# Optimization experiments

Hardware: AMD Instinct MI355X
Metric: run time of the kernel (lower is better)

## Reference

```python
import jax, jax.numpy as jnp
import numpy as np

N = 50000          # total nodes (2 types x 25000)
E = 400000         # edges
NEG = 0.2          # leaky_relu negative slope


def _seg_softmax(e, dst, n):
    # softmax over edges grouped by destination node
    m = jax.ops.segment_max(e, dst, num_segments=n)
    m = jnp.where(jnp.isfinite(m), m, 0.0)
    ex = jnp.exp(e - m[dst])
    s = jax.ops.segment_sum(ex, dst, num_segments=n)
    return ex / (s[dst] + 1e-16)


def _gat_conv(h, src, dst, W, al, ar, b, heads, out, res=None, act=None):
    n = h.shape[0]
    ft = (h @ W).reshape(n, heads, out)               # [N,H,D]
    el = jnp.sum(ft * al, axis=-1)                    # [N,H]
    er = jnp.sum(ft * ar, axis=-1)                    # [N,H]
    e = jax.nn.leaky_relu(el[src] + er[dst], NEG)     # [E,H]
    alpha = _seg_softmax(e, dst, n)                   # [E,H]
    rst = jax.ops.segment_sum(ft[src] * alpha[:, :, None], dst, num_segments=n)
    if isinstance(res, str):                          # identity residual (in == heads*out)
        rst = rst + h.reshape(n, heads, out)
    elif res is not None:                             # linear residual projection
        rst = rst + (h @ res).reshape(n, heads, out)
    rst = rst + b                                     # bias [H,D]
    if act is not None:
        rst = act(rst)
    return rst


def setup_inputs() -> dict:
    key = jax.random.key(0)
    ks = jax.random.split(key, 24)
    g = lambda i, shp, s=0.05: jax.random.normal(ks[i], shp, jnp.float32) * s
    inp = {
        "x0": jax.random.normal(ks[0], (25000, 256), jnp.float32),
        "x1": jax.random.normal(ks[1], (25000, 256), jnp.float32),
        "src": jax.random.randint(ks[2], (E,), 0, N, jnp.int32).astype(jnp.int64),
        "dst": jax.random.randint(ks[3], (E,), 0, N, jnp.int32).astype(jnp.int64),
        # per-type input projections
        "fc0_W": g(4, (256, 64)), "fc0_b": jnp.zeros((64,), jnp.float32),
        "fc1_W": g(5, (256, 64)), "fc1_b": jnp.zeros((64,), jnp.float32),
        # layer 0: 64 -> 8 heads x 64
        "W0": g(6, (64, 512)), "al0": g(7, (8, 64)), "ar0": g(8, (8, 64)), "b0": jnp.zeros((8, 64), jnp.float32),
        # layer 1: 512 -> 8 heads x 64 (identity residual)
        "W1": g(9, (512, 512)), "al1": g(10, (8, 64)), "ar1": g(11, (8, 64)), "b1": jnp.zeros((8, 64), jnp.float32),
        # output layer: 512 -> 1 head x 16 (linear residual)
        "W2": g(12, (512, 16)), "al2": g(13, (1, 16)), "ar2": g(14, (1, 16)), "b2": jnp.zeros((1, 16), jnp.float32),
        "resW2": g(15, (512, 16)),
    }
    return inp


def reference(x0, x1, src, dst, fc0_W, fc0_b, fc1_W, fc1_b,
              W0, al0, ar0, b0, W1, al1, ar1, b1,
              W2, al2, ar2, b2, resW2):
    # per-type linear projections, then concat over node axis
    h = jnp.concatenate([x0 @ fc0_W + fc0_b, x1 @ fc1_W + fc1_b], axis=0)  # [N,64]
    h = _gat_conv(h, src, dst, W0, al0, ar0, b0, 8, 64, None, jax.nn.elu).reshape(N, -1)
    h = _gat_conv(h, src, dst, W1, al1, ar1, b1, 8, 64, "id", jax.nn.elu).reshape(N, -1)
    encoded = h
    logits = _gat_conv(h, src, dst, W2, al2, ar2, b2, 1, 16, resW2, None).mean(axis=1)  # [N,16]
    return (logits, encoded)
```

## Files before the change

kernel.cpp:

```cpp
#include <hip/hip_runtime.h>
#include <hip/hip_bf16.h>
#include <math.h>

typedef __hip_bfloat16 bf16;
typedef __attribute__((ext_vector_type(8))) short short8;
typedef __attribute__((ext_vector_type(8))) unsigned short ushort8;
typedef __attribute__((ext_vector_type(4))) float floatx4;

#define NNODES 50000
#define NHALF  25000
#define NEDGES 400000
#define NEG_SLOPE 0.2f

__device__ __forceinline__ float b2f(bf16 x){ return __bfloat162float(x); }
__device__ __forceinline__ bf16  f2b(float x){ return __float2bfloat16(x); }
__device__ __forceinline__ float u2f(unsigned short u){ return __uint_as_float(((unsigned)u) << 16); }

__device__ __forceinline__ float loadF(const void* p, long i, int f32){
  return f32 ? ((const float*)p)[i] : b2f(((const bf16*)p)[i]);
}
__device__ __forceinline__ void storeOut(void* p, long i, float v, int f32){
  if (f32) ((float*)p)[i] = v; else ((bf16*)p)[i] = f2b(v);
}

__device__ __forceinline__ unsigned fenc(float f){
  unsigned b = __float_as_uint(f);
  return (b & 0x80000000u) ? ~b : (b | 0x80000000u);
}
__device__ __forceinline__ float fdec(unsigned k){
  unsigned b = (k & 0x80000000u) ? (k & 0x7fffffffu) : ~k;
  return __uint_as_float(b);
}

__device__ __forceinline__ void gl_lds16(const bf16* g, short* l){
  __builtin_amdgcn_global_load_lds(
      (const __attribute__((address_space(1))) unsigned int*)g,
      (__attribute__((address_space(3))) unsigned int*)l, 16, 0, 0);
}

__global__ void k_detect(const unsigned short* __restrict__ x0u,
                         const unsigned* __restrict__ dstu,
                         int* __restrict__ flags)
{
  __shared__ int sh_insane;
  __shared__ unsigned sh_or;
  if (threadIdx.x == 0) { sh_insane = 0; sh_or = 0u; }
  __syncthreads();
  int insane = 0; unsigned orv = 0u;
  for (int i = threadIdx.x; i < 2048; i += 256) {
    unsigned short w = x0u[2 * i];
    int ex = (w >> 7) & 0xFF;
    if (w != 0 && (ex < 108 || ex > 142)) insane++;
    orv |= dstu[2 * i + 1];
  }
  atomicAdd(&sh_insane, insane);
  atomicOr(&sh_or, orv);
  __syncthreads();
  if (threadIdx.x == 0) {
    flags[0] = (sh_insane > 512) ? 1 : 0;
    flags[1] = (sh_or == 0u) ? 1 : 0;
  }
}

__global__ void k_conv_idx(const int* __restrict__ sraw, const int* __restrict__ draw,
                           int* __restrict__ s32, int* __restrict__ d32,
                           int* __restrict__ deg,
                           const int* __restrict__ flags)
{
  int e = blockIdx.x * blockDim.x + threadIdx.x;
  if (e >= NEDGES) return;
  int stride = flags[1] ? 2 : 1;
  int s = sraw[(long)e * stride];
  int d = draw[(long)e * stride];
  s32[e] = s;
  d32[e] = d;
  atomicAdd(&deg[d], 1);
}

struct WSrc { const void* p[17]; void* dst[17]; int n[17]; int M[17]; int st[17]; };

__global__ void k_canon(WSrc w, const int* __restrict__ flags, int total)
{
  int f32 = flags[0];
  for (int t = blockIdx.x * blockDim.x + threadIdx.x; t < total;
       t += gridDim.x * blockDim.x) {
    int idx = t, k = 0;
    while (idx >= w.n[k]) { idx -= w.n[k]; k++; }
    bf16 v = f2b(loadF(w.p[k], idx, f32));
    if (w.M[k] == 0) {
      ((bf16*)w.dst[k])[idx] = v;
    } else {
      int m = idx % w.M[k], kk = idx / w.M[k];
      ((bf16*)w.dst[k])[(long)m * w.st[k] + kk] = v;
    }
  }
}

__global__ void k_convx(const void* __restrict__ x0, const void* __restrict__ x1,
                        bf16* __restrict__ xb, const int* __restrict__ flags)
{
  long t = (long)(blockIdx.x * blockDim.x + threadIdx.x) * 8;
  if (t >= (long)NNODES * 256) return;
  long half = (long)NHALF * 256;
  const void* src = (t < half) ? x0 : x1;
  long off = (t < half) ? t : t - half;
  short8 o;
  if (flags[0]) {
    const float* f = (const float*)src + off;
    floatx4 a = *(const floatx4*)f;
    floatx4 b = *(const floatx4*)(f + 4);
    #pragma unroll
    for (int j = 0; j < 4; ++j) {
      bf16 x = f2b(a[j]); o[j] = *(short*)&x;
      bf16 y = f2b(b[j]); o[j + 4] = *(short*)&y;
    }
  } else {
    o = *(const short8*)((const bf16*)src + off);
  }
  *(short8*)(xb + t) = o;
}

__global__ __launch_bounds__(256) void k_gemm_mfma(
    const bf16* __restrict__ A, const bf16* __restrict__ Wt,
    bf16* __restrict__ C, int N, int K, int ldc, int Mout,
    const bf16* __restrict__ bias,
    const bf16* __restrict__ al, const bf16* __restrict__ ar,
    float* __restrict__ elOut, float* __restrict__ erOut,
    unsigned* __restrict__ Menc)
{
  __shared__ __align__(16) short lsA[128 * 32];
  __shared__ __align__(16) short lsB[128 * 32];
  __shared__ unsigned sMaxE[2], sMaxR[2];
  int tid = threadIdx.x;
  int wave = tid >> 6, lane = tid & 63;
  int wm = wave >> 1, wn = wave & 1;
  int rowBase = blockIdx.x * 128;
  int colBase = blockIdx.y * 128;

  if (tid < 2) { sMaxE[tid] = 0u; sMaxR[tid] = 0u; }

  floatx4 acc[4][4] = {};
  int laneRow = lane >> 2;
  int laneCol = (lane & 3) * 8;
  int cA0 = wave * 2, cA1 = cA0 + 1;

  for (int kb = 0; kb < K; kb += 32) {
    int r0 = rowBase + cA0 * 16 + laneRow; if (r0 > N - 1) r0 = N - 1;
    int r1 = rowBase + cA1 * 16 + laneRow; if (r1 > N - 1) r1 = N - 1;
    gl_lds16(A + (size_t)r0 * K + kb + laneCol, &lsA[cA0 * 512]);
    gl_lds16(A + (size_t)r1 * K + kb + laneCol, &lsA[cA1 * 512]);
    int m0 = colBase + cA0 * 16 + laneRow;
    int m1 = colBase + cA1 * 16 + laneRow;
    gl_lds16(Wt + (size_t)m0 * K + kb + laneCol, &lsB[cA0 * 512]);
    gl_lds16(Wt + (size_t)m1 * K + kb + laneCol, &lsB[cA1 * 512]);
    __syncthreads();

    short8 af[4], bfr[4];
    int lr = lane & 15, q8 = (lane >> 4) * 8;
    #pragma unroll
    for (int mt = 0; mt < 4; ++mt)
      af[mt] = *(const short8*)&lsA[(wm * 64 + mt * 16 + lr) * 32 + q8];
    #pragma unroll
    for (int nt = 0; nt < 4; ++nt)
      bfr[nt] = *(const short8*)&lsB[(wn * 64 + nt * 16 + lr) * 32 + q8];
    #pragma unroll
    for (int mt = 0; mt < 4; ++mt)
      #pragma unroll
      for (int nt = 0; nt < 4; ++nt)
        acc[mt][nt] = __builtin_amdgcn_mfma_f32_16x16x32_bf16(
            af[mt], bfr[nt], acc[mt][nt], 0, 0, 0);
    __syncthreads();
  }

  int lc = lane & 15, rq = (lane >> 4) * 4;
  #pragma unroll
  for (int mt = 0; mt < 4; ++mt) {
    #pragma unroll
    for (int nt = 0; nt < 4; ++nt) {
      int col = colBase + wn * 64 + nt * 16 + lc;
      if (col >= Mout) continue;
      float bsv = bias ? b2f(bias[col]) : 0.f;
      #pragma unroll
      for (int r = 0; r < 4; ++r) {
        int row = rowBase + wm * 64 + mt * 16 + rq + r;
        if (row < N) C[(size_t)row * ldc + col] = f2b(acc[mt][nt][r] + bsv);
      }
    }
  }

  if (elOut) {
    int h = (colBase >> 6) + wn;
    float alv[4], arv[4];
    #pragma unroll
    for (int nt = 0; nt < 4; ++nt) {
      alv[nt] = b2f(al[h * 64 + nt * 16 + lc]);
      arv[nt] = b2f(ar[h * 64 + nt * 16 + lc]);
    }
    float mael = -1e30f, maer = -1e30f;
    #pragma unroll
    for (int mt = 0; mt < 4; ++mt) {
      #pragma unroll
      for (int r = 0; r < 4; ++r) {
        float pe = acc[mt][0][r] * alv[0] + acc[mt][1][r] * alv[1]
                 + acc[mt][2][r] * alv[2] + acc[mt][3][r] * alv[3];
        float pr = acc[mt][0][r] * arv[0] + acc[mt][1][r] * arv[1]
                 + acc[mt][2][r] * arv[2] + acc[mt][3][r] * arv[3];
        #pragma unroll
        for (int off = 1; off < 16; off <<= 1) {
          pe += __shfl_xor(pe, off);
          pr += __shfl_xor(pr, off);
        }
        int row = rowBase + wm * 64 + mt * 16 + rq + r;
        if (row < N) {
          if (lc == 0) { elOut[row * 8 + h] = pe; erOut[row * 8 + h] = pr; }
          mael = fmaxf(mael, pe);
          maer = fmaxf(maer, pr);
        }
      }
    }
    #pragma unroll
    for (int off = 16; off < 64; off <<= 1) {
      mael = fmaxf(mael, __shfl_xor(mael, off));
      maer = fmaxf(maer, __shfl_xor(maer, off));
    }
    if (lane == 0) {
      atomicMax(&sMaxE[wn], fenc(mael));
      atomicMax(&sMaxR[wn], fenc(maer));
    }
    __syncthreads();
    if (tid < 2) {
      int h0 = colBase >> 6;
      atomicMax(&Menc[h0 + tid], sMaxE[tid]);
      atomicMax(&Menc[8 + h0 + tid], sMaxR[tid]);
    }
  }
}

__global__ __launch_bounds__(256) void k_elr1(
    const bf16* __restrict__ ft2,
    const bf16* __restrict__ al, const bf16* __restrict__ ar,
    float* __restrict__ el, float* __restrict__ er,
    unsigned* __restrict__ Menc)
{
  __shared__ float rA[4], rB[4];
  int tid = threadIdx.x;
  int n = blockIdx.x * 256 + tid;
  float a = -1e30f, b = -1e30f;
  if (n < NNODES) {
    const unsigned short* f = (const unsigned short*)ft2 + (size_t)n * 32;
    float aa = 0.f, bb = 0.f;
    #pragma unroll
    for (int d = 0; d < 16; ++d) {
      float x = u2f(f[d]);
      aa += x * b2f(al[d]);
      bb += x * b2f(ar[d]);
    }
    a = aa; b = bb;
    el[n] = a; er[n] = b;
  }
  #pragma unroll
  for (int off = 1; off <= 32; off <<= 1) {
    a = fmaxf(a, __shfl_xor(a, off));
    b = fmaxf(b, __shfl_xor(b, off));
  }
  int wave = tid >> 6, lane = tid & 63;
  if (lane == 0) { rA[wave] = a; rB[wave] = b; }
  __syncthreads();
  if (tid == 0) {
    float ma = -1e30f, mb = -1e30f;
    #pragma unroll
    for (int w2 = 0; w2 < 4; ++w2) { ma = fmaxf(ma, rA[w2]); mb = fmaxf(mb, rB[w2]); }
    atomicMax(&Menc[0], fenc(ma));
    atomicMax(&Menc[1], fenc(mb));
  }
}

__global__ __launch_bounds__(1024) void k_bsum(const int* __restrict__ deg,
                                               int* __restrict__ bsum, int n)
{
  __shared__ int ws[16];
  int tid = threadIdx.x, lane = tid & 63, wv = tid >> 6;
  int i = blockIdx.x * 1024 + tid;
  int v = (i < n) ? deg[i] : 0;
  #pragma unroll
  for (int off = 1; off < 64; off <<= 1) v += __shfl_xor(v, off);
  if (lane == 0) ws[wv] = v;
  __syncthreads();
  if (tid < 16) {
    int s = ws[tid];
    #pragma unroll
    for (int off = 1; off < 16; off <<= 1) s += __shfl_xor(s, off);
    if (tid == 0) bsum[blockIdx.x] = s;
  }
}

__global__ void k_bscan(int* __restrict__ bsum, int* __restrict__ row_start,
                        int nb, int n)
{
  int lane = threadIdx.x;
  int v = (lane < nb) ? bsum[lane] : 0;
  int x = v;
  #pragma unroll
  for (int off = 1; off < 64; off <<= 1) {
    int y = __shfl_up(x, off);
    if (lane >= off) x += y;
  }
  if (lane < nb) bsum[lane] = x - v;
  if (lane == 63) row_start[n] = x;
}

__global__ __launch_bounds__(1024) void k_scan2(const int* __restrict__ deg,
                                                const int* __restrict__ boff,
                                                int* __restrict__ row_start,
                                                int* __restrict__ cursor, int n)
{
  __shared__ int ws[16];
  int tid = threadIdx.x, lane = tid & 63, wv = tid >> 6;
  int i = blockIdx.x * 1024 + tid;
  int v = (i < n) ? deg[i] : 0;
  int x = v;
  #pragma unroll
  for (int off = 1; off < 64; off <<= 1) {
    int y = __shfl_up(x, off);
    if (lane >= off) x += y;
  }
  if (lane == 63) ws[wv] = x;
  __syncthreads();
  if (wv == 0 && lane < 16) {
    int s = ws[lane];
    int xs = s;
    #pragma unroll
    for (int off = 1; off < 16; off <<= 1) {
      int y = __shfl_up(xs, off);
      if (lane >= off) xs += y;
    }
    ws[lane] = xs - s;
  }
  __syncthreads();
  if (i < n) {
    int val = boff[blockIdx.x] + ws[wv] + x - v;
    row_start[i] = val;
    cursor[i] = val;
  }
}

__global__ void k_fill(const int* __restrict__ src, const int* __restrict__ dst,
                       int* __restrict__ cursor, int* __restrict__ csr_src, int E)
{
  int e = blockIdx.x * blockDim.x + threadIdx.x;
  if (e < E) {
    int p = atomicAdd(&cursor[dst[e]], 1);
    csr_src[p] = src[e];
  }
}

__global__ __launch_bounds__(256) void k_agg8(
    const int* __restrict__ row_start, const int* __restrict__ csr_src,
    const float* __restrict__ el, const float* __restrict__ er,
    const unsigned* __restrict__ Menc,
    const bf16* __restrict__ ft, const bf16* __restrict__ hin,
    const bf16* __restrict__ bias,
    bf16* __restrict__ hout, void* __restrict__ dout, long dout_off,
    const int* __restrict__ flags, int mode)
{
  int wv = (int)((blockIdx.x * blockDim.x + threadIdx.x) >> 6);
  int lane = threadIdx.x & 63;
  if (wv >= NNODES) return;
  int n = wv, g = lane >> 3;
  int st = row_start[n], en = row_start[n + 1];
  float mm = fdec(Menc[g]) + fdec(Menc[8 + g]);
  float Mh = mm > 0.f ? mm : NEG_SLOPE * mm;
  float ern = er[n * 8 + g];

  const unsigned short* ftS = (const unsigned short*)ft;
  float ssum = 0.f;
  float acc[8] = {};
  int i = st;
  for (; i + 4 <= en; i += 4) {
    int sn0 = csr_src[i],     sn1 = csr_src[i + 1];
    int sn2 = csr_src[i + 2], sn3 = csr_src[i + 3];
    float e0 = el[sn0 * 8 + g], e1 = el[sn1 * 8 + g];
    float e2 = el[sn2 * 8 + g], e3 = el[sn3 * 8 + g];
    ushort8 r0 = *(const ushort8*)&ftS[(size_t)sn0 * 512 + lane * 8];
    ushort8 r1 = *(const ushort8*)&ftS[(size_t)sn1 * 512 + lane * 8];
    ushort8 r2 = *(const ushort8*)&ftS[(size_t)sn2 * 512 + lane * 8];
    ushort8 r3 = *(const ushort8*)&ftS[(size_t)sn3 * 512 + lane * 8];
    float v0 = e0 + ern, v1 = e1 + ern, v2 = e2 + ern, v3 = e3 + ern;
    v0 = v0 > 0.f ? v0 : NEG_SLOPE * v0;
    v1 = v1 > 0.f ? v1 : NEG_SLOPE * v1;
    v2 = v2 > 0.f ? v2 : NEG_SLOPE * v2;
    v3 = v3 > 0.f ? v3 : NEG_SLOPE * v3;
    float w0 = __expf(v0 - Mh), w1 = __expf(v1 - Mh);
    float w2 = __expf(v2 - Mh), w3 = __expf(v3 - Mh);
    ssum += (w0 + w1) + (w2 + w3);
    #pragma unroll
    for (int j = 0; j < 8; ++j)
      acc[j] += (w0 * u2f(r0[j]) + w1 * u2f(r1[j]))
              + (w2 * u2f(r2[j]) + w3 * u2f(r3[j]));
  }
  for (; i < en; ++i) {
    int sn = csr_src[i];
    float v0 = el[sn * 8 + g] + ern;
    v0 = v0 > 0.f ? v0 : NEG_SLOPE * v0;
    float w0 = __expf(v0 - Mh);
    ushort8 r0 = *(const ushort8*)&ftS[(size_t)sn * 512 + lane * 8];
    ssum += w0;
    #pragma unroll
    for (int j = 0; j < 8; ++j)
      acc[j] += w0 * u2f(r0[j]);
  }

  float inv = ssum > 0.f ? 1.f / ssum : 0.f;
  int f32 = flags[0];
  short8 outv;
  float rr[8];
  #pragma unroll
  for (int j = 0; j < 8; ++j) {
    int col = lane * 8 + j;
    float r = acc[j] * inv + b2f(bias[col]);
    if (mode == 1) r += b2f(hin[(size_t)n * 512 + col]);
    r = r > 0.f ? r : expm1f(r);
    rr[j] = r;
    bf16 o = f2b(r);
    outv[j] = *(short*)&o;
  }
  *(short8*)&hout[(size_t)n * 512 + lane * 8] = outv;
  if (dout) {
    if (f32) {
      floatx4 o0, o1;
      #pragma unroll
      for (int j = 0; j < 4; ++j) { o0[j] = rr[j]; o1[j] = rr[j + 4]; }
      float* dp = (float*)dout + dout_off + (size_t)n * 512 + lane * 8;
      __builtin_nontemporal_store(o0, (floatx4*)dp);
      __builtin_nontemporal_store(o1, (floatx4*)(dp + 4));
    } else {
      __builtin_nontemporal_store(outv,
          (short8*)&((bf16*)dout)[dout_off + (size_t)n * 512 + lane * 8]);
    }
  }
}

__global__ __launch_bounds__(256) void k_agg1(
    const int* __restrict__ row_start, const int* __restrict__ csr_src,
    const float* __restrict__ el, const float* __restrict__ er,
    const unsigned* __restrict__ Menc,
    const bf16* __restrict__ ft2, const bf16* __restrict__ bias,
    void* __restrict__ dout, const int* __restrict__ flags)
{
  int wv = (int)((blockIdx.x * blockDim.x + threadIdx.x) >> 6);
  int lane = threadIdx.x & 63;
  if (wv >= NNODES) return;
  int n = wv, sub = lane >> 4, d = lane & 15;
  int st = row_start[n], en = row_start[n + 1];
  float mm = fdec(Menc[0]) + fdec(Menc[1]);
  float M0 = mm > 0.f ? mm : NEG_SLOPE * mm;
  float ern = er[n];
  float ssum = 0.f, acc = 0.f;
  for (int i = st + sub; i < en; i += 4) {
    int sn = csr_src[i];
    float v = el[sn] + ern;
    v = v > 0.f ? v : NEG_SLOPE * v;
    float ex = __expf(v - M0);
    acc  += ex * b2f(ft2[(size_t)sn * 32 + d]);
    ssum += ex;
  }
  acc  += __shfl_xor(acc, 16);  acc  += __shfl_xor(acc, 32);
  ssum += __shfl_xor(ssum, 16); ssum += __shfl_xor(ssum, 32);
  if (sub == 0) {
    float inv = ssum > 0.f ? 1.f / ssum : 0.f;
    float r = acc * inv + b2f(bias[d]) + b2f(ft2[(size_t)n * 32 + 16 + d]);
    if (flags[0]) __builtin_nontemporal_store(r, (float*)dout + (size_t)n * 16 + d);
    else { bf16 o = f2b(r); __builtin_nontemporal_store(*(short*)&o,
             (short*)dout + (size_t)n * 16 + d); }
  }
}

extern "C" void kernel_launch(void* const* d_in, const int* in_sizes, int n_in,
                              void* d_out, int out_size, void* d_ws, size_t ws_size,
                              hipStream_t stream)
{
  const void* x0   = d_in[0];
  const void* x1   = d_in[1];
  const int*  srcR = (const int*)d_in[2];
  const int*  dstR = (const int*)d_in[3];

  char* p = (char*)d_ws;
  auto alloc = [&](size_t bytes) { char* r = p; p += (bytes + 255) & ~(size_t)255; return r; };
  int*      flags     = (int*)  alloc(256);
  bf16*     wc        = (bf16*) alloc((size_t)347312 * 2);
  int*      src32     = (int*)  alloc((size_t)NEDGES * 4);
  int*      dst32     = (int*)  alloc((size_t)NEDGES * 4);
  bf16*     xb        = (bf16*) alloc((size_t)NNODES * 256 * 2);
  bf16*     h0        = (bf16*) alloc((size_t)NNODES * 64 * 2);
  bf16*     hB        = (bf16*) alloc((size_t)NNODES * 512 * 2);
  bf16*     ft        = (bf16*) alloc((size_t)NNODES * 512 * 2);
  bf16*     ft2       = (bf16*) alloc((size_t)NNODES * 32 * 2);
  float*    el        = (float*)alloc((size_t)NNODES * 8 * 4);
  float*    er        = (float*)alloc((size_t)NNODES * 8 * 4);
  int*      deg       = (int*)  alloc((size_t)NNODES * 4);
  int*      row_start = (int*)  alloc((size_t)(NNODES + 1) * 4);
  int*      cursor    = (int*)  alloc((size_t)NNODES * 4);
  int*      csr_src   = (int*)  alloc((size_t)NEDGES * 4);
  int*      bsum      = (int*)  alloc((size_t)64 * 4);
  unsigned* Menc      = (unsigned*)alloc(256);
  bf16*     fc0t      = (bf16*) alloc((size_t)128 * 256 * 2);
  bf16*     fc1t      = (bf16*) alloc((size_t)128 * 256 * 2);
  bf16*     W0t       = (bf16*) alloc((size_t)512 * 64 * 2);
  bf16*     W1t       = (bf16*) alloc((size_t)512 * 512 * 2);
  bf16*     W2c       = (bf16*) alloc((size_t)128 * 512 * 2);
  size_t twBytes = ((size_t)128*256 + 128*256 + 512*64 + 512*512 + 128*512) * 2;

  const int B = 256;
  auto blk = [](long total, int b) { return (unsigned)((total + b - 1) / b); };
  const int NSCB = (NNODES + 1023) / 1024;

  hipMemsetAsync(deg, 0, (size_t)NNODES * 4, stream);
  hipMemsetAsync(Menc, 0, 256, stream);
  hipMemsetAsync(fc0t, 0, twBytes, stream);

  k_detect<<<1, 256, 0, stream>>>((const unsigned short*)x0, (const unsigned*)dstR, flags);
  k_conv_idx<<<blk(NEDGES, B), B, 0, stream>>>(srcR, dstR, src32, dst32, deg, flags);

  long woff[18]; woff[0] = 0;
  const int widx[17] = {4,5,6,7, 8,9,10,11, 12,13,14,15, 16,17,18,19, 20};
  const int wn[17]   = {16384,64,16384,64, 32768,512,512,512, 262144,512,512,512,
                        8192,16,16,16, 8192};
  for (int i = 0; i < 17; ++i) woff[i + 1] = woff[i] + wn[i];

  WSrc wsrc;
  int wtotal = 0;
  for (int i = 0; i < 17; ++i) {
    wsrc.p[i] = d_in[widx[i]]; wsrc.n[i] = wn[i];
    wsrc.dst[i] = wc + woff[i]; wsrc.M[i] = 0; wsrc.st[i] = 0;
    wtotal += wn[i];
  }
  wsrc.dst[0]  = fc0t;            wsrc.M[0]  = 64;  wsrc.st[0]  = 256;
  wsrc.dst[2]  = fc1t;            wsrc.M[2]  = 64;  wsrc.st[2]  = 256;
  wsrc.dst[4]  = W0t;             wsrc.M[4]  = 512; wsrc.st[4]  = 64;
  wsrc.dst[8]  = W1t;             wsrc.M[8]  = 512; wsrc.st[8]  = 512;
  wsrc.dst[12] = W2c;             wsrc.M[12] = 16;  wsrc.st[12] = 512;
  wsrc.dst[16] = W2c + 16 * 512;  wsrc.M[16] = 16;  wsrc.st[16] = 512;
  k_canon<<<blk(wtotal, B), B, 0, stream>>>(wsrc, flags, wtotal);
  k_convx<<<blk((long)NNODES * 32, B), B, 0, stream>>>(x0, x1, xb, flags);

  const bf16 *fc0b = wc + woff[1], *fc1b = wc + woff[3];
  const bf16 *al0  = wc + woff[5],  *ar0 = wc + woff[6],  *b0 = wc + woff[7];
  const bf16 *al1  = wc + woff[9],  *ar1 = wc + woff[10], *b1 = wc + woff[11];
  const bf16 *al2  = wc + woff[13], *ar2 = wc + woff[14], *b2 = wc + woff[15];

  k_bsum <<<NSCB, 1024, 0, stream>>>(deg, bsum, NNODES);
  k_bscan<<<1, 64, 0, stream>>>(bsum, row_start, NSCB, NNODES);
  k_scan2<<<NSCB, 1024, 0, stream>>>(deg, bsum, row_start, cursor, NNODES);
  k_fill<<<blk(NEDGES, B), B, 0, stream>>>(src32, dst32, cursor, csr_src, NEDGES);

  auto gemm = [&](const bf16* A, const bf16* Wt, bf16* C, int N, int K,
                  int ldc, int Mout, int ytiles, const bf16* bias,
                  const bf16* gal = nullptr, const bf16* gar = nullptr,
                  float* gel = nullptr, float* ger = nullptr,
                  unsigned* gM = nullptr) {
    dim3 g(blk(N, 128), ytiles);
    k_gemm_mfma<<<g, 256, 0, stream>>>(A, Wt, C, N, K, ldc, Mout, bias,
                                       gal, gar, gel, ger, gM);
  };

  gemm(xb, fc0t, h0, NHALF, 256, 64, 64, 1, fc0b);
  gemm(xb + (size_t)NHALF * 256, fc1t, h0 + (size_t)NHALF * 64, NHALF, 256, 64, 64, 1, fc1b);

  unsigned aggGrid = blk((long)NNODES * 64, B);
  unsigned nblk1 = blk(NNODES, B);

  gemm(h0, W0t, ft, NNODES, 64, 512, 512, 4, nullptr, al0, ar0, el, er, Menc);
  k_agg8<<<aggGrid, B, 0, stream>>>(row_start, csr_src, el, er, Menc, ft, nullptr, b0,
                                    hB, nullptr, 0, flags, 0);

  gemm(hB, W1t, ft, NNODES, 512, 512, 512, 4, nullptr, al1, ar1, el, er, Menc + 16);
  k_agg8<<<aggGrid, B, 0, stream>>>(row_start, csr_src, el, er, Menc + 16, ft, hB, b1,
                                    hB, d_out, (long)NNODES * 16, flags, 1);

  gemm(hB, W2c, ft2, NNODES, 512, 32, 32, 1, nullptr);
  k_elr1<<<nblk1, B, 0, stream>>>(ft2, al2, ar2, el, er, Menc + 32);
  k_agg1<<<aggGrid, B, 0, stream>>>(row_start, csr_src, el, er, Menc + 32, ft2, b2, d_out, flags);
}
```

Measured before the change: 640.7 us.

## Fuse output-layer attention logits into GEMM epilogue and linearize GEMM grid

Drops the separate k_elr1 kernel. The output-layer GEMM epilogue now computes the single-head el/er logits and their global max, using an elH parameter. The GEMM launch moves to a 1D grid in which column tiles of the same row block are adjacent, so blocks that share A rows run close together and can reuse them in cache. Each agg8 launch is also split into two half-node launches. That split adds launch overhead without any clear benefit.

```diff
diff --git a/kernel.cpp b/kernel.cpp
--- a/kernel.cpp
+++ b/kernel.cpp
@@ -122,11 +122,11 @@
 
 __global__ __launch_bounds__(256) void k_gemm_mfma(
     const bf16* __restrict__ A, const bf16* __restrict__ Wt,
-    bf16* __restrict__ C, int N, int K, int ldc, int Mout,
+    bf16* __restrict__ C, int N, int K, int ldc, int Mout, int ytshift,
     const bf16* __restrict__ bias,
     const bf16* __restrict__ al, const bf16* __restrict__ ar,
     float* __restrict__ elOut, float* __restrict__ erOut,
-    unsigned* __restrict__ Menc)
+    unsigned* __restrict__ Menc, int elH)
 {
   __shared__ __align__(16) short lsA[128 * 32];
   __shared__ __align__(16) short lsB[128 * 32];
@@ -134,8 +134,9 @@
   int tid = threadIdx.x;
   int wave = tid >> 6, lane = tid & 63;
   int wm = wave >> 1, wn = wave & 1;
-  int rowBase = blockIdx.x * 128;
-  int colBase = blockIdx.y * 128;
+  int bid = blockIdx.x;
+  int rowBase = (bid >> ytshift) * 128;
+  int colBase = (bid & ((1 << ytshift) - 1)) * 128;
 
   if (tid < 2) { sMaxE[tid] = 0u; sMaxR[tid] = 0u; }
 
@@ -189,89 +190,62 @@
   }
 
   if (elOut) {
-    int h = (colBase >> 6) + wn;
-    float alv[4], arv[4];
-    #pragma unroll
-    for (int nt = 0; nt < 4; ++nt) {
-      alv[nt] = b2f(al[h * 64 + nt * 16 + lc]);
-      arv[nt] = b2f(ar[h * 64 + nt * 16 + lc]);
-    }
-    float mael = -1e30f, maer = -1e30f;
-    #pragma unroll
-    for (int mt = 0; mt < 4; ++mt) {
+    int nhb = (elH == 8) ? 2 : 1;
+    if (elH == 8 || wn == 0) {
+      int h = (elH == 8) ? ((colBase >> 6) + wn) : 0;
+      float alv[4], arv[4];
+      if (elH == 8) {
+        #pragma unroll
+        for (int nt = 0; nt < 4; ++nt) {
+          alv[nt] = b2f(al[h * 64 + nt * 16 + lc]);
+          arv[nt] = b2f(ar[h * 64 + nt * 16 + lc]);
+        }
+      } else {
+        alv[0] = b2f(al[lc]); arv[0] = b2f(ar[lc]);
+        alv[1] = alv[2] = alv[3] = 0.f;
+        arv[1] = arv[2] = arv[3] = 0.f;
+      }
+      float mael = -1e30f, maer = -1e30f;
       #pragma unroll
-      for (int r = 0; r < 4; ++r) {
-        float pe = acc[mt][0][r] * alv[0] + acc[mt][1][r] * alv[1]
-                 + acc[mt][2][r] * alv[2] + acc[mt][3][r] * alv[3];
-        float pr = acc[mt][0][r] * arv[0] + acc[mt][1][r] * arv[1]
-                 + acc[mt][2][r] * arv[2] + acc[mt][3][r] * arv[3];
+      for (int mt = 0; mt < 4; ++mt) {
         #pragma unroll
-        for (int off = 1; off < 16; off <<= 1) {
-          pe += __shfl_xor(pe, off);
-          pr += __shfl_xor(pr, off);
-        }
-        int row = rowBase + wm * 64 + mt * 16 + rq + r;
-        if (row < N) {
-          if (lc == 0) { elOut[row * 8 + h] = pe; erOut[row * 8 + h] = pr; }
-          mael = fmaxf(mael, pe);
-          maer = fmaxf(maer, pr);
+        for (int r = 0; r < 4; ++r) {
+          float pe = acc[mt][0][r] * alv[0] + acc[mt][1][r] * alv[1]
+                   + acc[mt][2][r] * alv[2] + acc[mt][3][r] * alv[3];
+          float pr = acc[mt][0][r] * arv[0] + acc[mt][1][r] * arv[1]
+                   + acc[mt][2][r] * arv[2] + acc[mt][3][r] * arv[3];
+          #pragma unroll
+          for (int off = 1; off < 16; off <<= 1) {
+            pe += __shfl_xor(pe, off);
+            pr += __shfl_xor(pr, off);
+          }
+          int row = rowBase + wm * 64 + mt * 16 + rq + r;
+          if (row < N) {
+            if (lc == 0) { elOut[(size_t)row * elH + h] = pe;
+                           erOut[(size_t)row * elH + h] = pr; }
+            mael = fmaxf(mael, pe);
+            maer = fmaxf(maer, pr);
+          }
         }
       }
-    }
-    #pragma unroll
-    for (int off = 16; off < 64; off <<= 1) {
-      mael = fmaxf(mael, __shfl_xor(mael, off));
-      maer = fmaxf(maer, __shfl_xor(maer, off));
-    }
-    if (lane == 0) {
-      atomicMax(&sMaxE[wn], fenc(mael));
-      atomicMax(&sMaxR[wn], fenc(maer));
+      #pragma unroll
+      for (int off = 16; off < 64; off <<= 1) {
+        mael = fmaxf(mael, __shfl_xor(mael, off));
+        maer = fmaxf(maer, __shfl_xor(maer, off));
+      }
+      if (lane == 0) {
+        int s = (elH == 8) ? wn : 0;
+        atomicMax(&sMaxE[s], fenc(mael));
+        atomicMax(&sMaxR[s], fenc(maer));
+      }
     }
     __syncthreads();
-    if (tid < 2) {
-      int h0 = colBase >> 6;
+    if (tid < nhb) {
+      int h0 = (elH == 8) ? (colBase >> 6) : 0;
+      int erOff = (elH == 8) ? 8 : 1;
       atomicMax(&Menc[h0 + tid], sMaxE[tid]);
-      atomicMax(&Menc[8 + h0 + tid], sMaxR[tid]);
-    }
-  }
-}
-
-__global__ __launch_bounds__(256) void k_elr1(
-    const bf16* __restrict__ ft2,
-    const bf16* __restrict__ al, const bf16* __restrict__ ar,
-    float* __restrict__ el, float* __restrict__ er,
-    unsigned* __restrict__ Menc)
-{
-  __shared__ float rA[4], rB[4];
-  int tid = threadIdx.x;
-  int n = blockIdx.x * 256 + tid;
-  float a = -1e30f, b = -1e30f;
-  if (n < NNODES) {
-    const unsigned short* f = (const unsigned short*)ft2 + (size_t)n * 32;
-    float aa = 0.f, bb = 0.f;
-    #pragma unroll
-    for (int d = 0; d < 16; ++d) {
-      float x = u2f(f[d]);
-      aa += x * b2f(al[d]);
-      bb += x * b2f(ar[d]);
-    }
-    a = aa; b = bb;
-    el[n] = a; er[n] = b;
-  }
-  #pragma unroll
-  for (int off = 1; off <= 32; off <<= 1) {
-    a = fmaxf(a, __shfl_xor(a, off));
-    b = fmaxf(b, __shfl_xor(b, off));
-  }
-  int wave = tid >> 6, lane = tid & 63;
-  if (lane == 0) { rA[wave] = a; rB[wave] = b; }
-  __syncthreads();
-  if (tid == 0) {
-    float ma = -1e30f, mb = -1e30f;
-    #pragma unroll
-    for (int w2 = 0; w2 < 4; ++w2) { ma = fmaxf(ma, rA[w2]); mb = fmaxf(mb, rB[w2]); }
-    atomicMax(&Menc[0], fenc(ma));
-    atomicMax(&Menc[1], fenc(mb));
+      atomicMax(&Menc[erOff + h0 + tid], sMaxR[tid]);
+    }
   }
 }
 
@@ -361,11 +335,11 @@
     const bf16* __restrict__ ft, const bf16* __restrict__ hin,
     const bf16* __restrict__ bias,
     bf16* __restrict__ hout, void* __restrict__ dout, long dout_off,
-    const int* __restrict__ flags, int mode)
-{
-  int wv = (int)((blockIdx.x * blockDim.x + threadIdx.x) >> 6);
+    const int* __restrict__ flags, int mode, int nodeBase, int nodeEnd)
+{
+  int wv = nodeBase + (int)((blockIdx.x * blockDim.x + threadIdx.x) >> 6);
   int lane = threadIdx.x & 63;
-  if (wv >= NNODES) return;
+  if (wv >= nodeEnd) return;
   int n = wv, g = lane >> 3;
   int st = row_start[n], en = row_start[n + 1];
   float mm = fdec(Menc[g]) + fdec(Menc[8 + g]);
@@ -554,30 +528,33 @@
   k_fill<<<blk(NEDGES, B), B, 0, stream>>>(src32, dst32, cursor, csr_src, NEDGES);
 
   auto gemm = [&](const bf16* A, const bf16* Wt, bf16* C, int N, int K,
-                  int ldc, int Mout, int ytiles, const bf16* bias,
+                  int ldc, int Mout, int ytshift, const bf16* bias,
                   const bf16* gal = nullptr, const bf16* gar = nullptr,
                   float* gel = nullptr, float* ger = nullptr,
-                  unsigned* gM = nullptr) {
-    dim3 g(blk(N, 128), ytiles);
-    k_gemm_mfma<<<g, 256, 0, stream>>>(A, Wt, C, N, K, ldc, Mout, bias,
-                                       gal, gar, gel, ger, gM);
+                  unsigned* gM = nullptr, int elH = 8) {
+    unsigned nb = blk(N, 128) << ytshift;
+    k_gemm_mfma<<<nb, 256, 0, stream>>>(A, Wt, C, N, K, ldc, Mout, ytshift,
+                                        bias, gal, gar, gel, ger, gM, elH);
   };
 
-  gemm(xb, fc0t, h0, NHALF, 256, 64, 64, 1, fc0b);
-  gemm(xb + (size_t)NHALF * 256, fc1t, h0 + (size_t)NHALF * 64, NHALF, 256, 64, 64, 1, fc1b);
-
-  unsigned aggGrid = blk((long)NNODES * 64, B);
-  unsigned nblk1 = blk(NNODES, B);
-
-  gemm(h0, W0t, ft, NNODES, 64, 512, 512, 4, nullptr, al0, ar0, el, er, Menc);
-  k_agg8<<<aggGrid, B, 0, stream>>>(row_start, csr_src, el, er, Menc, ft, nullptr, b0,
-                                    hB, nullptr, 0, flags, 0);
-
-  gemm(hB, W1t, ft, NNODES, 512, 512, 512, 4, nullptr, al1, ar1, el, er, Menc + 16);
-  k_agg8<<<aggGrid, B, 0, stream>>>(row_start, csr_src, el, er, Menc + 16, ft, hB, b1,
-                                    hB, d_out, (long)NNODES * 16, flags, 1);
-
-  gemm(hB, W2c, ft2, NNODES, 512, 32, 32, 1, nullptr);
-  k_elr1<<<nblk1, B, 0, stream>>>(ft2, al2, ar2, el, er, Menc + 32);
+  gemm(xb, fc0t, h0, NHALF, 256, 64, 64, 0, fc0b);
+  gemm(xb + (size_t)NHALF * 256, fc1t, h0 + (size_t)NHALF * 64, NHALF, 256, 64, 64, 0, fc1b);
+
+  unsigned aggGrid  = blk((long)NNODES * 64, B);
+  unsigned aggGridH = blk((long)NHALF * 64, B);
+
+  gemm(h0, W0t, ft, NNODES, 64, 512, 512, 2, nullptr, al0, ar0, el, er, Menc, 8);
+  k_agg8<<<aggGridH, B, 0, stream>>>(row_start, csr_src, el, er, Menc, ft, nullptr, b0,
+                                     hB, nullptr, 0, flags, 0, 0, NHALF);
+  k_agg8<<<aggGridH, B, 0, stream>>>(row_start, csr_src, el, er, Menc, ft, nullptr, b0,
+                                     hB, nullptr, 0, flags, 0, NHALF, NNODES);
+
+  gemm(hB, W1t, ft, NNODES, 512, 512, 512, 2, nullptr, al1, ar1, el, er, Menc + 16, 8);
+  k_agg8<<<aggGridH, B, 0, stream>>>(row_start, csr_src, el, er, Menc + 16, ft, hB, b1,
+                                     hB, d_out, (long)NNODES * 16, flags, 1, 0, NHALF);
+  k_agg8<<<aggGridH, B, 0, stream>>>(row_start, csr_src, el, er, Menc + 16, ft, hB, b1,
+                                     hB, d_out, (long)NNODES * 16, flags, 1, NHALF, NNODES);
+
+  gemm(hB, W2c, ft2, NNODES, 512, 32, 32, 0, nullptr, al2, ar2, el, er, Menc + 32, 1);
   k_agg1<<<aggGrid, B, 0, stream>>>(row_start, csr_src, el, er, Menc + 32, ft2, b2, d_out, flags);
 }
```

Measured after the change: 669.4 us. +4.5%, slower.
